# Kernel optimization log

Hardware: AMD Instinct MI355X
Metric: run time of the kernel (lower is better)

## Reference

```python
import jax, jax.numpy as jnp
import numpy as np

FLOAT4_E2M1_MAX = 6.0
FLOAT8_E4M3_MAX = 448.0
BLOCK = 16  # nvfp4 micro-block size


def _round_to_fp(x, mant_bits, min_exp, max_val):
    """Round x to nearest value representable in a tiny float format
    (sign + exponent + mant_bits mantissa, min normal exponent min_exp,
    gradual underflow below it, saturate at max_val)."""
    a = jnp.abs(x)
    e = jnp.floor(jnp.log2(jnp.where(a > 0, a, 1.0)))
    e = jnp.maximum(e, float(min_exp))
    step = jnp.exp2(e - mant_bits)  # quantization step at this exponent
    q = jnp.minimum(jnp.round(a / step) * step, max_val)
    return jnp.sign(x) * q


def nvfp4_fake_quant(x):
    """NVFP4 quantize-dequantize: global fp32 scale, per-16-elem fp8-e4m3
    block scales, fp4-e2m1 values. Matches ops.scaled_fp4_quant math."""
    amax = jnp.max(jnp.abs(x)).astype(jnp.float32)
    gscale = FLOAT8_E4M3_MAX * FLOAT4_E2M1_MAX / amax
    shp = x.shape
    xr = x.reshape(shp[:-1] + (shp[-1] // BLOCK, BLOCK))
    bmax = jnp.max(jnp.abs(xr), axis=-1, keepdims=True)
    # block scale encoded in fp8-e4m3 (3 mantissa bits, min exp -6, max 448)
    sc = _round_to_fp(bmax / FLOAT4_E2M1_MAX * gscale, 3, -6, FLOAT8_E4M3_MAX) / gscale
    sc_safe = jnp.where(sc > 0, sc, 1.0)
    # fp4-e2m1 values: {0, .5, 1, 1.5, 2, 3, 4, 6} (1 mantissa bit, min exp 0, max 6)
    xq = _round_to_fp(xr / sc_safe, 1, 0, FLOAT4_E2M1_MAX) * sc
    return xq.reshape(shp)


def setup_inputs() -> dict:
    key = jax.random.key(0)
    kx, kw, kb = jax.random.split(key, 3)
    x = jax.random.normal(kx, (4, 2048, 4096), dtype=jnp.float32)
    W = jax.random.normal(kw, (4096, 4096), dtype=jnp.float32) * 0.02
    b = jax.random.normal(kb, (4096,), dtype=jnp.float32) * 0.01
    return {"x": x, "W": W, "b": b}


def reference(x, W, b):
    xq = nvfp4_fake_quant(x)   # a_bit=4 activation quant
    Wq = nvfp4_fake_quant(W)   # w_bit=4 weight quant
    # F.linear(x_q, qweight_fp, bias): [b,s,k] @ [n,k]^T + [n]
    return jnp.einsum('bsk,nk->bsn', xq, Wq) + b
```

## Files before the change

kernel.cpp:

```cpp
#include <hip/hip_runtime.h>
#include <hip/hip_bf16.h>
#include <stdint.h>


#define GM 8192
#define GN 4096
#define GK 4096

#define BM 256
#define BN 256
#define BK 64
#define NT (GK / BK)

typedef short bf16x8 __attribute__((ext_vector_type(8)));
typedef float f32x4 __attribute__((ext_vector_type(4)));

__device__ __forceinline__ float round_tiny(float x, int mant_bits, int min_exp, float max_val) {
  float a = fabsf(x);
  if (a == 0.0f) return 0.0f;
  int e = (int)((__float_as_uint(a) >> 23) & 0xFFu) - 127;
  if (e < min_exp) e = min_exp;
  float s_up = __int_as_float((unsigned)(mant_bits - e + 127) << 23);
  float s_dn = __int_as_float((unsigned)(e - mant_bits + 127) << 23);
  float q = fminf(rintf(a * s_up) * s_dn, max_val);
  return copysignf(q, x);
}

__global__ void amax_part(const float4* __restrict__ src, int n4, float* __restrict__ part) {
  float m = 0.0f;
  int stride = gridDim.x * blockDim.x;
  for (int i = blockIdx.x * blockDim.x + threadIdx.x; i < n4; i += stride) {
    float4 v = src[i];
    m = fmaxf(m, fmaxf(fmaxf(fabsf(v.x), fabsf(v.y)), fmaxf(fabsf(v.z), fabsf(v.w))));
  }
#pragma unroll
  for (int off = 32; off > 0; off >>= 1) m = fmaxf(m, __shfl_xor(m, off, 64));
  __shared__ float sm[4];
  int wave = threadIdx.x >> 6;
  if ((threadIdx.x & 63) == 0) sm[wave] = m;
  __syncthreads();
  if (threadIdx.x == 0)
    part[blockIdx.x] = fmaxf(fmaxf(sm[0], sm[1]), fmaxf(sm[2], sm[3]));
}

__global__ void amax_final(const float* __restrict__ px, const float* __restrict__ pw,
                           unsigned int* __restrict__ amax2) {
  int t = threadIdx.x;
  float mx = fmaxf(px[t], px[t + 512]);
  float mw = pw[t];
#pragma unroll
  for (int off = 32; off > 0; off >>= 1) {
    mx = fmaxf(mx, __shfl_xor(mx, off, 64));
    mw = fmaxf(mw, __shfl_xor(mw, off, 64));
  }
  __shared__ float sx[8], sw[8];
  int wave = t >> 6;
  if ((t & 63) == 0) { sx[wave] = mx; sw[wave] = mw; }
  __syncthreads();
  if (t == 0) {
    float ax = sx[0], aw = sw[0];
#pragma unroll
    for (int i = 1; i < 8; ++i) { ax = fmaxf(ax, sx[i]); aw = fmaxf(aw, sw[i]); }
    amax2[0] = __float_as_uint(ax);
    amax2[1] = __float_as_uint(aw);
  }
}

__global__ void quant_kernel(const float* __restrict__ src, unsigned short* __restrict__ dst,
                             const unsigned int* __restrict__ amax_bits, int nblk) {
  const float amax = __uint_as_float(amax_bits[0]);
  const float gscale = 2688.0f / amax;
  int stride = gridDim.x * blockDim.x;
  for (int i = blockIdx.x * blockDim.x + threadIdx.x; i < nblk; i += stride) {
    const float4* p = (const float4*)src + (size_t)i * 4;
    float4 v0 = p[0], v1 = p[1], v2 = p[2], v3 = p[3];
    float vals[16] = {v0.x, v0.y, v0.z, v0.w, v1.x, v1.y, v1.z, v1.w,
                      v2.x, v2.y, v2.z, v2.w, v3.x, v3.y, v3.z, v3.w};
    float bmax = 0.0f;
#pragma unroll
    for (int j = 0; j < 16; ++j) bmax = fmaxf(bmax, fabsf(vals[j]));
    float sc8 = round_tiny(bmax / 6.0f * gscale, 3, -6, 448.0f);
    unsigned short o[16];
    if (sc8 > 0.0f) {
      float sc = sc8 / gscale;
#pragma unroll
      for (int j = 0; j < 16; ++j) {
        float q = round_tiny(vals[j] / sc, 1, 0, 6.0f);
        float d = q * sc8;
        unsigned u = __float_as_uint(d);
        u += 0x7FFFu + ((u >> 16) & 1u);
        o[j] = (unsigned short)(u >> 16);
      }
    } else {
#pragma unroll
      for (int j = 0; j < 16; ++j) o[j] = 0;
    }
    uint4* dq = (uint4*)(dst + (size_t)i * 16);
    const uint4* oq = (const uint4*)o;
    dq[0] = oq[0];
    dq[1] = oq[1];
  }
}

__global__ __launch_bounds__(512, 2) void gemm256(
    const unsigned short* __restrict__ A,
    const unsigned short* __restrict__ Bt,
    const float* __restrict__ bias,
    const unsigned int* __restrict__ amax2,
    float* __restrict__ C) {
  __shared__ char lds[131072];
  char* As = lds;
  char* Bs = lds + 65536;
  const int tid = threadIdx.x;
  const int lane = tid & 63;
  const int wave = tid >> 6;

  const int nwg = gridDim.x * gridDim.y;
  int id = blockIdx.y * gridDim.x + blockIdx.x;
  int swz = (id & 7) * (nwg >> 3) + (id >> 3);
  const int brow = (swz / gridDim.x) * BM;
  const int bcol = (swz % gridDim.x) * BN;

  const int wr = (wave >> 2) * 128;
  const int wc = (wave & 3) * 64;

  f32x4 acc[8][4] = {};

  int ldsb[2], gA[2], gB[2];
#pragma unroll
  for (int j = 0; j < 2; ++j) {
    int L0 = (j * 8 + wave) * 1024;
    int L = L0 + lane * 16;
    int row = ((L >> 7) << 1) | ((L >> 6) & 1);
    int cb = ((L >> 4) & 3) ^ ((L >> 7) & 3);
    ldsb[j] = L0;
    gA[j] = (brow + row) * GK + cb * 8;
    gB[j] = (bcol + row) * GK + cb * 8;
  }

  int offA[8], offB[4];
#pragma unroll
  for (int m = 0; m < 8; ++m) {
    int row = wr + m * 16 + (lane & 15);
    offA[m] = ((row >> 1) << 7) + ((row & 1) << 6) + ((((lane >> 4) & 3) ^ ((row >> 1) & 3)) << 4);
  }
#pragma unroll
  for (int n = 0; n < 4; ++n) {
    int row = wc + n * 16 + (lane & 15);
    offB[n] = ((row >> 1) << 7) + ((row & 1) << 6) + ((((lane >> 4) & 3) ^ ((row >> 1) & 3)) << 4);
  }

  auto stage = [&](int s) {
    if (s >= 4 * NT) return;
    int tau = s >> 2, r = s & 3;
    int kh = r >> 1;
    int kt = tau * BK + kh * 32;
    char* slot = ((r & 1) ? Bs : As) + ((((tau & 1) << 1) + kh) << 14);
    const unsigned short* op = (r & 1) ? Bt : A;
    const int* g = (r & 1) ? gB : gA;
#pragma unroll
    for (int j = 0; j < 2; ++j) {
      const unsigned short* src = op + (size_t)(g[j] + kt);
      __builtin_amdgcn_global_load_lds(
          (__attribute__((address_space(1))) void*)src,
          (__attribute__((address_space(3))) void*)(slot + ldsb[j]),
          16, 0, 0);
    }
  };

  for (int s = 0; s < 5; ++s) stage(s);

  for (int t = 0; t < NT; ++t) {
    if (t == NT - 1)
      asm volatile("s_waitcnt vmcnt(0)" ::: "memory");
    else
      asm volatile("s_waitcnt vmcnt(2)" ::: "memory");
    asm volatile("s_barrier" ::: "memory");

    char* At0 = As + (((t & 1) << 1) << 14);
    char* Bt0 = Bs + (((t & 1) << 1) << 14);
#pragma unroll
    for (int ksub = 0; ksub < 2; ++ksub) {
      const char* Aslot = At0 + (ksub << 14);
      const char* Bslot = Bt0 + (ksub << 14);
      bf16x8 a[8], b0, b1;
#pragma unroll
      for (int m = 0; m < 8; ++m) a[m] = *(const bf16x8*)(Aslot + offA[m]);
      b0 = *(const bf16x8*)(Bslot + offB[0]);
      b1 = *(const bf16x8*)(Bslot + offB[1]);
      stage(4 * t + ksub * 2 + 5);
      asm volatile("s_barrier" ::: "memory");
      asm volatile("s_waitcnt lgkmcnt(0)" ::: "memory");
      __builtin_amdgcn_sched_barrier(0);
      __builtin_amdgcn_s_setprio(1);
#pragma unroll
      for (int m = 0; m < 8; ++m) {
        acc[m][0] = __builtin_amdgcn_mfma_f32_16x16x32_bf16(a[m], b0, acc[m][0], 0, 0, 0);
        acc[m][1] = __builtin_amdgcn_mfma_f32_16x16x32_bf16(a[m], b1, acc[m][1], 0, 0, 0);
      }
      __builtin_amdgcn_s_setprio(0);
      asm volatile("s_barrier" ::: "memory");
      b0 = *(const bf16x8*)(Bslot + offB[2]);
      b1 = *(const bf16x8*)(Bslot + offB[3]);
      stage(4 * t + ksub * 2 + 6);
      asm volatile("s_barrier" ::: "memory");
      asm volatile("s_waitcnt lgkmcnt(0)" ::: "memory");
      __builtin_amdgcn_sched_barrier(0);
      __builtin_amdgcn_s_setprio(1);
#pragma unroll
      for (int m = 0; m < 8; ++m) {
        acc[m][2] = __builtin_amdgcn_mfma_f32_16x16x32_bf16(a[m], b0, acc[m][2], 0, 0, 0);
        acc[m][3] = __builtin_amdgcn_mfma_f32_16x16x32_bf16(a[m], b1, acc[m][3], 0, 0, 0);
      }
      __builtin_amdgcn_s_setprio(0);
      asm volatile("s_barrier" ::: "memory");
    }
  }

  const float ax = __uint_as_float(amax2[0]);
  const float aw = __uint_as_float(amax2[1]);
  const float inv = 1.0f / ((2688.0f / ax) * (2688.0f / aw));
#pragma unroll
  for (int m = 0; m < 8; ++m) {
    int row0 = brow + wr + m * 16 + ((lane >> 4) << 2);
#pragma unroll
    for (int n = 0; n < 4; ++n) {
      int col = bcol + wc + n * 16 + (lane & 15);
      float bb = bias[col];
#pragma unroll
      for (int j = 0; j < 4; ++j)
        C[(size_t)(row0 + j) * GN + col] = acc[m][n][j] * inv + bb;
    }
  }
}

extern "C" void kernel_launch(void* const* d_in, const int* in_sizes, int n_in,
                              void* d_out, int out_size, void* d_ws, size_t ws_size,
                              hipStream_t stream) {
  const float* x = (const float*)d_in[0];
  const float* W = (const float*)d_in[1];
  const float* b = (const float*)d_in[2];
  float* out = (float*)d_out;

  unsigned int* amax2 = (unsigned int*)d_ws;
  float* px = (float*)((char*)d_ws + 256);
  float* pw = (float*)((char*)d_ws + 8192);
  unsigned short* Aq = (unsigned short*)((char*)d_ws + 65536);
  unsigned short* Bq = Aq + (size_t)GM * GK;

  amax_part<<<1024, 256, 0, stream>>>((const float4*)x, GM * GK / 4, px);
  amax_part<<<512, 256, 0, stream>>>((const float4*)W, GN * GK / 4, pw);
  amax_final<<<1, 512, 0, stream>>>(px, pw, amax2);
  quant_kernel<<<2048, 256, 0, stream>>>(x, Aq, amax2, GM * GK / 16);
  quant_kernel<<<2048, 256, 0, stream>>>(W, Bq, amax2 + 1, GN * GK / 16);
  dim3 grid(GN / BN, GM / BM);
  gemm256<<<grid, 512, 0, stream>>>(Aq, Bq, b, amax2, out);
}
```

Measured before the change: 529.6 us.

## Merge amax and quant launches for x and W, fold final reduce into quant

Result: no change. 528.3 us (-0.2%).

```diff
diff --git a/kernel.cpp b/kernel.cpp
--- a/kernel.cpp
+++ b/kernel.cpp
@@ -26,79 +26,79 @@
   return copysignf(q, x);
 }
 
-__global__ void amax_part(const float4* __restrict__ src, int n4, float* __restrict__ part) {
+__device__ __forceinline__ unsigned short pack_bf16(float d) {
+  unsigned u = __float_as_uint(d);
+  u += 0x7FFFu + ((u >> 16) & 1u);
+  return (unsigned short)(u >> 16);
+}
+
+__global__ void amax_part2(const float4* __restrict__ x4, int nx4,
+                           const float4* __restrict__ w4, int nw4,
+                           float* __restrict__ px, float* __restrict__ pw) {
+  const int b = blockIdx.x;
+  const bool isX = b < 1024;
+  const float4* src = isX ? x4 : w4;
+  const int n4 = isX ? nx4 : nw4;
+  const int bb = isX ? b : b - 1024;
+  const int nb = isX ? 1024 : 512;
   float m = 0.0f;
-  int stride = gridDim.x * blockDim.x;
-  for (int i = blockIdx.x * blockDim.x + threadIdx.x; i < n4; i += stride) {
+  const int stride = nb * 256;
+  for (int i = bb * 256 + threadIdx.x; i < n4; i += stride) {
     float4 v = src[i];
     m = fmaxf(m, fmaxf(fmaxf(fabsf(v.x), fabsf(v.y)), fmaxf(fabsf(v.z), fabsf(v.w))));
   }
 #pragma unroll
   for (int off = 32; off > 0; off >>= 1) m = fmaxf(m, __shfl_xor(m, off, 64));
   __shared__ float sm[4];
-  int wave = threadIdx.x >> 6;
-  if ((threadIdx.x & 63) == 0) sm[wave] = m;
+  if ((threadIdx.x & 63) == 0) sm[threadIdx.x >> 6] = m;
   __syncthreads();
   if (threadIdx.x == 0)
-    part[blockIdx.x] = fmaxf(fmaxf(sm[0], sm[1]), fmaxf(sm[2], sm[3]));
-}
-
-__global__ void amax_final(const float* __restrict__ px, const float* __restrict__ pw,
-                           unsigned int* __restrict__ amax2) {
-  int t = threadIdx.x;
-  float mx = fmaxf(px[t], px[t + 512]);
-  float mw = pw[t];
-#pragma unroll
-  for (int off = 32; off > 0; off >>= 1) {
-    mx = fmaxf(mx, __shfl_xor(mx, off, 64));
-    mw = fmaxf(mw, __shfl_xor(mw, off, 64));
-  }
-  __shared__ float sx[8], sw[8];
-  int wave = t >> 6;
-  if ((t & 63) == 0) { sx[wave] = mx; sw[wave] = mw; }
+    (isX ? px : pw)[bb] = fmaxf(fmaxf(sm[0], sm[1]), fmaxf(sm[2], sm[3]));
+}
+
+__global__ void quant2(const float* __restrict__ x, const float* __restrict__ W,
+                       const float* __restrict__ px, const float* __restrict__ pw,
+                       unsigned short* __restrict__ Aq, unsigned short* __restrict__ Bq,
+                       unsigned int* __restrict__ amax2) {
+  const int tid = threadIdx.x;
+  const bool isX = blockIdx.x < 2048;
+  const float4* src = (const float4*)(isX ? x : W);
+  ushort4* dst = (ushort4*)(isX ? Aq : Bq);
+  const float* part = isX ? px : pw;
+  const int pcnt = isX ? 1024 : 512;
+  const int bb = isX ? blockIdx.x : blockIdx.x - 2048;
+  const int nb = isX ? 2048 : 1024;
+  const int n4 = isX ? (GM * GK / 4) : (GN * GK / 4);
+
+  float m = 0.0f;
+  for (int j = tid; j < pcnt; j += 256) m = fmaxf(m, part[j]);
+#pragma unroll
+  for (int off = 32; off > 0; off >>= 1) m = fmaxf(m, __shfl_xor(m, off, 64));
+  __shared__ float sm[4];
+  if ((tid & 63) == 0) sm[tid >> 6] = m;
   __syncthreads();
-  if (t == 0) {
-    float ax = sx[0], aw = sw[0];
-#pragma unroll
-    for (int i = 1; i < 8; ++i) { ax = fmaxf(ax, sx[i]); aw = fmaxf(aw, sw[i]); }
-    amax2[0] = __float_as_uint(ax);
-    amax2[1] = __float_as_uint(aw);
-  }
-}
-
-__global__ void quant_kernel(const float* __restrict__ src, unsigned short* __restrict__ dst,
-                             const unsigned int* __restrict__ amax_bits, int nblk) {
-  const float amax = __uint_as_float(amax_bits[0]);
+  const float amax = fmaxf(fmaxf(sm[0], sm[1]), fmaxf(sm[2], sm[3]));
+  if (bb == 0 && tid == 0) amax2[isX ? 0 : 1] = __float_as_uint(amax);
+
   const float gscale = 2688.0f / amax;
-  int stride = gridDim.x * blockDim.x;
-  for (int i = blockIdx.x * blockDim.x + threadIdx.x; i < nblk; i += stride) {
-    const float4* p = (const float4*)src + (size_t)i * 4;
-    float4 v0 = p[0], v1 = p[1], v2 = p[2], v3 = p[3];
-    float vals[16] = {v0.x, v0.y, v0.z, v0.w, v1.x, v1.y, v1.z, v1.w,
-                      v2.x, v2.y, v2.z, v2.w, v3.x, v3.y, v3.z, v3.w};
-    float bmax = 0.0f;
-#pragma unroll
-    for (int j = 0; j < 16; ++j) bmax = fmaxf(bmax, fabsf(vals[j]));
-    float sc8 = round_tiny(bmax / 6.0f * gscale, 3, -6, 448.0f);
-    unsigned short o[16];
+  const int stride = nb * 256;
+  for (int i = bb * 256 + tid; i < n4; i += stride) {
+    float4 v = src[i];
+    float a = fmaxf(fmaxf(fabsf(v.x), fabsf(v.y)), fmaxf(fabsf(v.z), fabsf(v.w)));
+    a = fmaxf(a, __shfl_xor(a, 1, 64));
+    a = fmaxf(a, __shfl_xor(a, 2, 64));
+    float sc8 = round_tiny(a / 6.0f * gscale, 3, -6, 448.0f);
+    ushort4 o;
     if (sc8 > 0.0f) {
       float sc = sc8 / gscale;
-#pragma unroll
-      for (int j = 0; j < 16; ++j) {
-        float q = round_tiny(vals[j] / sc, 1, 0, 6.0f);
-        float d = q * sc8;
-        unsigned u = __float_as_uint(d);
-        u += 0x7FFFu + ((u >> 16) & 1u);
-        o[j] = (unsigned short)(u >> 16);
-      }
+      o.x = pack_bf16(round_tiny(v.x / sc, 1, 0, 6.0f) * sc8);
+      o.y = pack_bf16(round_tiny(v.y / sc, 1, 0, 6.0f) * sc8);
+      o.z = pack_bf16(round_tiny(v.z / sc, 1, 0, 6.0f) * sc8);
+      o.w = pack_bf16(round_tiny(v.w / sc, 1, 0, 6.0f) * sc8);
     } else {
-#pragma unroll
-      for (int j = 0; j < 16; ++j) o[j] = 0;
-    }
-    uint4* dq = (uint4*)(dst + (size_t)i * 16);
-    const uint4* oq = (const uint4*)o;
-    dq[0] = oq[0];
-    dq[1] = oq[1];
+      o.x = o.y = o.z = o.w = 0;
+    }
+    dst[i] = o;
   }
 }
 
@@ -248,11 +248,9 @@
   unsigned short* Aq = (unsigned short*)((char*)d_ws + 65536);
   unsigned short* Bq = Aq + (size_t)GM * GK;
 
-  amax_part<<<1024, 256, 0, stream>>>((const float4*)x, GM * GK / 4, px);
-  amax_part<<<512, 256, 0, stream>>>((const float4*)W, GN * GK / 4, pw);
-  amax_final<<<1, 512, 0, stream>>>(px, pw, amax2);
-  quant_kernel<<<2048, 256, 0, stream>>>(x, Aq, amax2, GM * GK / 16);
-  quant_kernel<<<2048, 256, 0, stream>>>(W, Bq, amax2 + 1, GN * GK / 16);
+  amax_part2<<<1536, 256, 0, stream>>>((const float4*)x, GM * GK / 4,
+                                       (const float4*)W, GN * GK / 4, px, pw);
+  quant2<<<3072, 256, 0, stream>>>(x, W, px, pw, Aq, Bq, amax2);
   dim3 grid(GN / BN, GM / BM);
   gemm256<<<grid, 512, 0, stream>>>(Aq, Bq, b, amax2, out);
 }
```
